# Kernel optimization log

Measured on AMD Instinct MI355X. Metric: run time of the kernel, lower is better.

## Reference

```python
import jax, jax.numpy as jnp
import numpy as np

B, N, D = 256, 196, 1024   # batch, regions, vis_embed_dim
HID, ATT, SIN, WID, ISD = 1024, 256, 1024, 1024, 256
S = 10                      # sentence steps


def _lin(key, out_dim, in_dim):
    kw, kb = jax.random.split(key)
    w = jax.random.normal(kw, (out_dim, in_dim), jnp.float32) * 0.02
    b = jax.random.normal(kb, (out_dim,), jnp.float32) * 0.02
    return w, b


def setup_inputs() -> dict:
    key = jax.random.key(0)
    ks = jax.random.split(key, 16)
    inp = {}
    inp['vis_enc'] = jax.random.normal(ks[0], (B, N, D), jnp.float32)
    inp['sentences'] = jax.random.randint(ks[1], (B, S, 50), 0, 10000, jnp.int64)
    inp['enc_att_w'], inp['enc_att_b'] = _lin(ks[2], ATT, D)
    inp['dec_att_w'], inp['dec_att_b'] = _lin(ks[3], ATT, HID)
    inp['full_att_w'], inp['full_att_b'] = _lin(ks[4], 1, ATT)
    inp['ctx_w'], inp['ctx_b'] = _lin(ks[5], SIN, D)
    inp['W_ih'], inp['b_ih'] = _lin(ks[6], 4 * HID, SIN)
    inp['W_hh'], inp['b_hh'] = _lin(ks[7], 4 * HID, HID)
    inp['topic_hid_w'], inp['topic_hid_b'] = _lin(ks[8], WID, HID)
    inp['topic_ctx_w'], inp['topic_ctx_b'] = _lin(ks[9], WID, SIN)
    inp['stop_prev_w'], inp['stop_prev_b'] = _lin(ks[10], ISD, HID)
    inp['stop_cur_w'], inp['stop_cur_b'] = _lin(ks[11], ISD, HID)
    inp['final_stop_w'], inp['final_stop_b'] = _lin(ks[12], 2, ISD)
    return inp


def reference(vis_enc, sentences,
              enc_att_w, enc_att_b, dec_att_w, dec_att_b, full_att_w, full_att_b,
              ctx_w, ctx_b, W_ih, b_ih, W_hh, b_hh,
              topic_hid_w, topic_hid_b, topic_ctx_w, topic_ctx_b,
              stop_prev_w, stop_prev_b, stop_cur_w, stop_cur_b,
              final_stop_w, final_stop_b):
    batch, hid = vis_enc.shape[0], W_hh.shape[1]
    sent_num = sentences.shape[1]
    # encoder projection is h-independent -> hoist out of the recurrence
    vis_enc_att = jnp.einsum('bnd,ad->bna', vis_enc, enc_att_w) + enc_att_b  # [B,N,ATT]

    def step(carry, _):
        h, c = carry
        # CoAtt additive attention
        dec = h @ dec_att_w.T + dec_att_b                       # [B,ATT]
        join = jnp.tanh(vis_enc_att + dec[:, None, :])          # [B,N,ATT]
        logits = jnp.einsum('bna,a->bn', join, full_att_w[0]) + full_att_b[0]
        scores = jax.nn.softmax(logits, axis=1)                 # [B,N]
        att_out = jnp.einsum('bn,bnd->bd', scores, vis_enc)     # [B,D]
        ctx = att_out @ ctx_w.T + ctx_b                         # [B,SIN]
        h_prev = h
        # LSTMCell
        gates = ctx @ W_ih.T + b_ih + h @ W_hh.T + b_hh         # [B,4H]
        i, f, g, o = jnp.split(gates, 4, axis=1)
        c_new = jax.nn.sigmoid(f) * c + jax.nn.sigmoid(i) * jnp.tanh(g)
        h_new = jax.nn.sigmoid(o) * jnp.tanh(c_new)
        # topic + stop heads
        topic = jnp.tanh(h_new @ topic_hid_w.T + topic_hid_b
                         + ctx @ topic_ctx_w.T + topic_ctx_b)   # [B,WID]
        p = jnp.tanh(h_prev @ stop_prev_w.T + stop_prev_b
                     + h_new @ stop_cur_w.T + stop_cur_b)
        p = p @ final_stop_w.T + final_stop_b                   # [B,2]
        return (h_new, c_new), (topic, p)

    h0 = jnp.zeros((batch, hid), vis_enc.dtype)
    c0 = jnp.zeros((batch, hid), vis_enc.dtype)
    _, (topics, ps) = jax.lax.scan(step, (h0, c0), None, length=sent_num)
    topics = jnp.transpose(topics, (1, 0, 2))  # [B,S,WID]
    ps = jnp.transpose(ps, (1, 0, 2))          # [B,S,2]
    return topics, ps
```

## Files before the change

kernel.cpp:

```cpp
#include <hip/hip_runtime.h>
#include <hip/hip_bf16.h>
#include <math.h>

static constexpr int BB = 256;
static constexpr int NR = 196;
static constexpr int DV = 1024;
static constexpr int HH = 1024;
static constexpr int AT = 256;
static constexpr int SI = 1024;
static constexpr int WI = 1024;
static constexpr int IS = 256;
static constexpr int ST = 10;

__device__ __forceinline__ float sigmoidf_(float x) { return 1.0f / (1.0f + expf(-x)); }

__device__ __forceinline__ ushort f2bf(float x) {
    uint u = __float_as_uint(x);
    return (ushort)((u + 0x7FFFu + ((u >> 16) & 1u)) >> 16);
}
__device__ __forceinline__ float bf2f(ushort b) { return __uint_as_float(((uint)b) << 16); }

using bf16x8 = __attribute__((ext_vector_type(8))) short;
using f32x4  = __attribute__((ext_vector_type(4))) float;
#define MFMA_B16(a, b, c) __builtin_amdgcn_mfma_f32_16x16x32_bf16((a), (b), (c), 0, 0, 0)

__device__ __forceinline__ void split8(const float4& u, const float4& v, uint4& hq, uint4& lq) {
    ushort h0 = f2bf(u.x), h1 = f2bf(u.y), h2 = f2bf(u.z), h3 = f2bf(u.w);
    ushort h4 = f2bf(v.x), h5 = f2bf(v.y), h6 = f2bf(v.z), h7 = f2bf(v.w);
    hq.x = h0 | ((uint)h1 << 16); hq.y = h2 | ((uint)h3 << 16);
    hq.z = h4 | ((uint)h5 << 16); hq.w = h6 | ((uint)h7 << 16);
    ushort l0 = f2bf(u.x - bf2f(h0)), l1 = f2bf(u.y - bf2f(h1));
    ushort l2 = f2bf(u.z - bf2f(h2)), l3 = f2bf(u.w - bf2f(h3));
    ushort l4 = f2bf(v.x - bf2f(h4)), l5 = f2bf(v.y - bf2f(h5));
    ushort l6 = f2bf(v.z - bf2f(h6)), l7 = f2bf(v.w - bf2f(h7));
    lq.x = l0 | ((uint)l1 << 16); lq.y = l2 | ((uint)l3 << 16);
    lq.z = l4 | ((uint)l5 << 16); lq.w = l6 | ((uint)l7 << 16);
}

struct CvtTab { const float* s[9]; ushort* h[9]; ushort* l[9]; };

__global__ __launch_bounds__(256) void convert_split(CvtTab tab) {
    const int cum[10] = {0, 256, 512, 1536, 5632, 9728, 10752, 11776, 12032, 12288};
    const int bid = blockIdx.x;
    int seg = 0;
#pragma unroll
    for (int i = 1; i < 9; ++i) if (bid >= cum[i]) seg = i;
    const float* s = tab.s[seg];
    ushort* h = tab.h[seg];
    ushort* l = tab.l[seg];
    const int r = bid - cum[seg];
    int rd = r;
    if (seg == 3 || seg == 4) rd = (r & 1023) * 4 + (r >> 10);
    const int src = r * 1024 + threadIdx.x * 4;
    const size_t dst = (size_t)rd * 1024 + threadIdx.x * 4;
    float4 v = *(const float4*)(s + src);
    ushort h0 = f2bf(v.x), h1 = f2bf(v.y), h2 = f2bf(v.z), h3 = f2bf(v.w);
    uint2 hq, lq;
    hq.x = h0 | ((uint)h1 << 16); hq.y = h2 | ((uint)h3 << 16);
    ushort l0 = f2bf(v.x - bf2f(h0)), l1 = f2bf(v.y - bf2f(h1));
    ushort l2 = f2bf(v.z - bf2f(h2)), l3 = f2bf(v.w - bf2f(h3));
    lq.x = l0 | ((uint)l1 << 16); lq.y = l2 | ((uint)l3 << 16);
    *(uint2*)(h + dst) = hq;
    *(uint2*)(l + dst) = lq;
}

__global__ __launch_bounds__(256) void convert_vis(
    const float* __restrict__ src, ushort* __restrict__ dst)
{
    const size_t i = ((size_t)blockIdx.x * 256 + threadIdx.x) * 8;
    const float4 v0 = *(const float4*)(src + i);
    const float4 v1 = *(const float4*)(src + i + 4);
    uint4 o;
    o.x = f2bf(v0.x) | ((uint)f2bf(v0.y) << 16);
    o.y = f2bf(v0.z) | ((uint)f2bf(v0.w) << 16);
    o.z = f2bf(v1.x) | ((uint)f2bf(v1.y) << 16);
    o.w = f2bf(v1.z) | ((uint)f2bf(v1.w) << 16);
    *(uint4*)(dst + i) = o;
}

__global__ __launch_bounds__(256) void transpose_split(
    const float* __restrict__ src, ushort* __restrict__ dh, ushort* __restrict__ dl)
{
    __shared__ float T[32][33];
    const int tx = threadIdx.x & 31, ty = threadIdx.x >> 5;
    const int k0 = blockIdx.x * 32, n0 = blockIdx.y * 32;
#pragma unroll
    for (int j = 0; j < 4; ++j)
        T[ty + 8 * j][tx] = src[(size_t)(k0 + ty + 8 * j) * 1024 + n0 + tx];
    __syncthreads();
#pragma unroll
    for (int j = 0; j < 4; ++j) {
        const float v = T[tx][ty + 8 * j];
        const ushort h = f2bf(v);
        const size_t o = (size_t)(n0 + ty + 8 * j) * 1024 + k0 + tx;
        dh[o] = h;
        dl[o] = f2bf(v - bf2f(h));
    }
}

__global__ __launch_bounds__(256) void foldbias(
    const float* __restrict__ W, const float* __restrict__ v,
    const float* __restrict__ b, float* __restrict__ out)
{
    const int n = blockIdx.x * 4 + (threadIdx.x >> 6);
    const int lane = threadIdx.x & 63;
    const float* wr = W + (size_t)n * 1024;
    float p = 0.f;
#pragma unroll
    for (int i = 0; i < 4; ++i) {
        const float4 wv = *(const float4*)&wr[i * 256 + lane * 4];
        const float4 vv = *(const float4*)&v[i * 256 + lane * 4];
        p = fmaf(wv.x, vv.x, p); p = fmaf(wv.y, vv.y, p);
        p = fmaf(wv.z, vv.z, p); p = fmaf(wv.w, vv.w, p);
    }
    for (int off = 32; off; off >>= 1) p += __shfl_down(p, off);
    if (lane == 0) out[n] = p + b[n];
}

template <int ILV>
__global__ __launch_bounds__(256) void mgemm_ws(
    const float* __restrict__ A, const ushort* __restrict__ Wh, const ushort* __restrict__ Wl,
    ushort* __restrict__ Ch, ushort* __restrict__ Cl, int N, int K)
{
    __shared__ __align__(16) ushort SM[4 * 64 * 40];
    ushort* Ah = SM; ushort* Al = SM + 2560; ushort* Bh = SM + 5120; ushort* Bl = SM + 7680;

    const int t = threadIdx.x;
    const int m0 = blockIdx.y * 64, n0 = blockIdx.x * 64;
    const int w = t >> 6, lane = t & 63;
    const int l15 = lane & 15, q = lane >> 4;
    const int sr = t >> 2, sq = (t & 3) * 8;
    const int nch = K >> 5;

    f32x4 acc[4] = {};
    float4 pa0, pa1; uint4 pbh, pbl;
    auto pref = [&](int c) {
        const int k0 = c << 5;
        const float* ap = &A[(size_t)(m0 + sr) * K + k0 + sq];
        pa0 = *(const float4*)ap;
        pa1 = *(const float4*)(ap + 4);
        pbh = *(const uint4*)&Wh[(size_t)(n0 + sr) * K + k0 + sq];
        pbl = *(const uint4*)&Wl[(size_t)(n0 + sr) * K + k0 + sq];
    };
    pref(0);

    for (int c = 0; c < nch; ++c) {
        __syncthreads();
        uint4 hq, lq; split8(pa0, pa1, hq, lq);
        *(uint4*)&Ah[sr * 40 + sq] = hq;
        *(uint4*)&Al[sr * 40 + sq] = lq;
        *(uint4*)&Bh[sr * 40 + sq] = pbh;
        *(uint4*)&Bl[sr * 40 + sq] = pbl;
        __syncthreads();
        if (c + 1 < nch) pref(c + 1);
        const bf16x8 bh = *(const bf16x8*)&Bh[(w * 16 + l15) * 40 + q * 8];
        const bf16x8 bl = *(const bf16x8*)&Bl[(w * 16 + l15) * 40 + q * 8];
#pragma unroll
        for (int mi = 0; mi < 4; ++mi) {
            const bf16x8 ah = *(const bf16x8*)&Ah[(mi * 16 + l15) * 40 + q * 8];
            const bf16x8 al = *(const bf16x8*)&Al[(mi * 16 + l15) * 40 + q * 8];
            acc[mi] = MFMA_B16(ah, bh, acc[mi]);
            acc[mi] = MFMA_B16(ah, bl, acc[mi]);
            acc[mi] = MFMA_B16(al, bh, acc[mi]);
        }
    }

    const int col = n0 + w * 16 + l15;
#pragma unroll
    for (int mi = 0; mi < 4; ++mi) {
#pragma unroll
        for (int j = 0; j < 4; ++j) {
            const int row = m0 + mi * 16 + q * 4 + j;
            const int ro = ILV ? ((row & 1023) * 4 + (row >> 10)) : row;
            const float v = acc[mi][j];
            const ushort h = f2bf(v);
            Ch[(size_t)ro * N + col] = h;
            Cl[(size_t)ro * N + col] = f2bf(v - bf2f(h));
        }
    }
}

template <int EPI, int DUAL, int OMAP>
__global__ __launch_bounds__(256) void mgemm(
    const float* __restrict__ A1, const ushort* __restrict__ W1h, const ushort* __restrict__ W1l,
    const float* __restrict__ b1,
    const float* __restrict__ A2, const ushort* __restrict__ W2h, const ushort* __restrict__ W2l,
    const float* __restrict__ b2,
    float* __restrict__ C, int M, int N, int K, int ldc)
{
    __shared__ __align__(16) ushort SM[4 * 64 * 40];
    ushort* Ah = SM; ushort* Al = SM + 2560; ushort* Bh = SM + 5120; ushort* Bl = SM + 7680;

    const int t = threadIdx.x;
    const int m0 = blockIdx.y * 64, n0 = blockIdx.x * 64;
    const int w = t >> 6, lane = t & 63;
    const int l15 = lane & 15, q = lane >> 4;
    const int sr = t >> 2, sq = (t & 3) * 8;
    const int KC = K >> 5, nch = (DUAL ? 2 : 1) * KC;

    f32x4 acc[4] = {};
    float4 pa0, pa1; uint4 pbh, pbl;

    auto pref = [&](int c) {
        const int pass = DUAL ? (c >= KC ? 1 : 0) : 0;
        const int k0 = (c - pass * KC) << 5;
        const float* A = pass ? A2 : A1;
        const ushort* Wh = pass ? W2h : W1h;
        const ushort* Wl = pass ? W2l : W1l;
        const float* ap = &A[(size_t)(m0 + sr) * K + k0 + sq];
        pa0 = *(const float4*)ap;
        pa1 = *(const float4*)(ap + 4);
        pbh = *(const uint4*)&Wh[(size_t)(n0 + sr) * K + k0 + sq];
        pbl = *(const uint4*)&Wl[(size_t)(n0 + sr) * K + k0 + sq];
    };
    pref(0);

    for (int c = 0; c < nch; ++c) {
        __syncthreads();
        uint4 hq, lq; split8(pa0, pa1, hq, lq);
        *(uint4*)&Ah[sr * 40 + sq] = hq;
        *(uint4*)&Al[sr * 40 + sq] = lq;
        *(uint4*)&Bh[sr * 40 + sq] = pbh;
        *(uint4*)&Bl[sr * 40 + sq] = pbl;
        __syncthreads();
        if (c + 1 < nch) pref(c + 1);
        const bf16x8 bh = *(const bf16x8*)&Bh[(w * 16 + l15) * 40 + q * 8];
        const bf16x8 bl = *(const bf16x8*)&Bl[(w * 16 + l15) * 40 + q * 8];
#pragma unroll
        for (int mi = 0; mi < 4; ++mi) {
            const bf16x8 ah = *(const bf16x8*)&Ah[(mi * 16 + l15) * 40 + q * 8];
            const bf16x8 al = *(const bf16x8*)&Al[(mi * 16 + l15) * 40 + q * 8];
            acc[mi] = MFMA_B16(ah, bh, acc[mi]);
            acc[mi] = MFMA_B16(ah, bl, acc[mi]);
            acc[mi] = MFMA_B16(al, bh, acc[mi]);
        }
    }

    const int col = n0 + w * 16 + l15;
    float bias = b1[col];
    if (DUAL) bias += b2[col];
#pragma unroll
    for (int mi = 0; mi < 4; ++mi) {
#pragma unroll
        for (int j = 0; j < 4; ++j) {
            const int row = m0 + mi * 16 + q * 4 + j;
            float v = acc[mi][j] + bias;
            if (EPI == 1) v = tanhf(v);
            if (OMAP)
                C[((size_t)(row & 255) * ST + (row >> 8)) * ldc + col] = v;
            else
                C[(size_t)row * ldc + col] = v;
        }
    }
}

__global__ __launch_bounds__(512) void mgemm8_lstm(
    const float* __restrict__ A1, const ushort* __restrict__ W1h, const ushort* __restrict__ W1l,
    const float* __restrict__ b1,
    const float* __restrict__ A2, const ushort* __restrict__ W2h, const ushort* __restrict__ W2l,
    const float* __restrict__ b2,
    int K, float* __restrict__ cvec, float* __restrict__ hnew)
{
    __shared__ __align__(16) ushort SM[32256];

    const int t = threadIdx.x;
    const int m0 = blockIdx.y * 64, n0 = blockIdx.x * 32;
    const int w = t >> 6, lane = t & 63;
    const int g = w >> 2, wg = w & 3;
    const int l15 = lane & 15, q = lane >> 4;
    const int tl = t & 255;
    const int sr = tl >> 2, sq4 = (tl & 3) * 16;
    const int br = tl >> 3, bq = (tl & 7) * 8;
    const int mh = wg >> 1;
    const int colL = (wg & 1) * 16 + l15;

    ushort* Ah = SM + g * 13824;
    ushort* Al = Ah + 4608;
    ushort* Bh = Al + 4608;
    ushort* Bl = Bh + 2304;

    const int nchg = K >> 6;
    const float*  A  = g ? A2 : A1;
    const ushort* Wh = g ? W2h : W1h;
    const ushort* Wl = g ? W2l : W1l;

    f32x4 acc[2] = {};
    float4 pa0, pa1, pa2, pa3; uint4 pbh, pbl;
    auto pref = [&](int c) {
        const int k0 = c << 6;
        const float* ap = &A[(size_t)(m0 + sr) * K + k0 + sq4];
        pa0 = *(const float4*)ap;       pa1 = *(const float4*)(ap + 4);
        pa2 = *(const float4*)(ap + 8); pa3 = *(const float4*)(ap + 12);
        pbh = *(const uint4*)&Wh[(size_t)(n0 + br) * K + k0 + bq];
        pbl = *(const uint4*)&Wl[(size_t)(n0 + br) * K + k0 + bq];
    };
    pref(0);

    for (int c = 0; c < nchg; ++c) {
        __syncthreads();
        uint4 hq, lq;
        split8(pa0, pa1, hq, lq);
        *(uint4*)&Ah[sr * 72 + sq4] = hq;
        *(uint4*)&Al[sr * 72 + sq4] = lq;
        split8(pa2, pa3, hq, lq);
        *(uint4*)&Ah[sr * 72 + sq4 + 8] = hq;
        *(uint4*)&Al[sr * 72 + sq4 + 8] = lq;
        *(uint4*)&Bh[br * 72 + bq] = pbh;
        *(uint4*)&Bl[br * 72 + bq] = pbl;
        __syncthreads();
        if (c + 1 < nchg) pref(c + 1);
#pragma unroll
        for (int ks = 0; ks < 2; ++ks) {
            const bf16x8 bh = *(const bf16x8*)&Bh[colL * 72 + ks * 32 + q * 8];
            const bf16x8 bl = *(const bf16x8*)&Bl[colL * 72 + ks * 32 + q * 8];
#pragma unroll
            for (int i = 0; i < 2; ++i) {
                const int mi = mh * 2 + i;
                const bf16x8 ah = *(const bf16x8*)&Ah[(mi * 16 + l15) * 72 + ks * 32 + q * 8];
                const bf16x8 al = *(const bf16x8*)&Al[(mi * 16 + l15) * 72 + ks * 32 + q * 8];
                acc[i] = MFMA_B16(ah, bh, acc[i]);
                acc[i] = MFMA_B16(ah, bl, acc[i]);
                acc[i] = MFMA_B16(al, bh, acc[i]);
            }
        }
    }

    float* comb = (float*)(SM + 27648);
    __syncthreads();
    if (g == 1) {
#pragma unroll
        for (int i = 0; i < 2; ++i)
#pragma unroll
            for (int j = 0; j < 4; ++j) comb[tl * 9 + i * 4 + j] = acc[i][j];
    }
    __syncthreads();
    if (g == 0) {
#pragma unroll
        for (int i = 0; i < 2; ++i)
#pragma unroll
            for (int j = 0; j < 4; ++j) acc[i][j] += comb[tl * 9 + i * 4 + j];
    }

    float* G = (float*)(SM + 13824);
    if (g == 0) {
        const int colG = n0 + colL;
        const int gate = colG & 3, unit = colG >> 2;
        const float bias = b1[gate * 1024 + unit] + b2[gate * 1024 + unit];
#pragma unroll
        for (int i = 0; i < 2; ++i) {
            const int mi = mh * 2 + i;
#pragma unroll
            for (int j = 0; j < 4; ++j)
                G[(mi * 16 + q * 4 + j) * 40 + colL] = acc[i][j] + bias;
        }
    }
    __syncthreads();
    {
        const int row = t >> 3, ul = t & 7;
        const float4 g4 = *(const float4*)&G[row * 40 + ul * 4];
        const size_t ci = (size_t)(m0 + row) * HH + (n0 >> 2) + ul;
        const float cn = sigmoidf_(g4.y) * cvec[ci] + sigmoidf_(g4.x) * tanhf(g4.z);
        cvec[ci] = cn;
        hnew[ci] = sigmoidf_(g4.w) * tanhf(cn);
    }
}

__global__ __launch_bounds__(256) void mgemm_preb(
    const ushort* __restrict__ vh, const ushort* __restrict__ Wh, const ushort* __restrict__ Wl,
    const float* __restrict__ bias, ushort* __restrict__ C)
{
    __shared__ __align__(16) ushort Avh[64 * 40];
    __shared__ __align__(16) ushort Bh[256 * 40];
    __shared__ __align__(16) ushort Bl[256 * 40];

    const int t = threadIdx.x;
    const int m0 = blockIdx.x * 64;
    const int w = t >> 6, lane = t & 63;
    const int l15 = lane & 15, q = lane >> 4;
    const int ar = t >> 2, ac = (t & 3) * 8;
    const int K = DV;

    f32x4 acc[4][4] = {};

    for (int c = 0; c < 32; ++c) {
        const int k0 = c << 5;
        __syncthreads();
        *(uint4*)&Avh[ar * 40 + ac] = *(const uint4*)&vh[(size_t)(m0 + ar) * K + k0 + ac];
#pragma unroll
        for (int j = 0; j < 4; ++j) {
            const int r = j * 64 + (t >> 2);
            *(uint4*)&Bh[r * 40 + ac] = *(const uint4*)&Wh[(size_t)r * K + k0 + ac];
            *(uint4*)&Bl[r * 40 + ac] = *(const uint4*)&Wl[(size_t)r * K + k0 + ac];
        }
        __syncthreads();

        bf16x8 ah[4];
#pragma unroll
        for (int mi = 0; mi < 4; ++mi)
            ah[mi] = *(const bf16x8*)&Avh[(mi * 16 + l15) * 40 + q * 8];
#pragma unroll
        for (int ni = 0; ni < 4; ++ni) {
            const bf16x8 bh = *(const bf16x8*)&Bh[(w * 64 + ni * 16 + l15) * 40 + q * 8];
            const bf16x8 bl = *(const bf16x8*)&Bl[(w * 64 + ni * 16 + l15) * 40 + q * 8];
#pragma unroll
            for (int mi = 0; mi < 4; ++mi) {
                acc[mi][ni] = MFMA_B16(ah[mi], bh, acc[mi][ni]);
                acc[mi][ni] = MFMA_B16(ah[mi], bl, acc[mi][ni]);
            }
        }
    }

#pragma unroll
    for (int ni = 0; ni < 4; ++ni) {
        const int col = w * 64 + ni * 16 + l15;
        const float bb = bias[col];
#pragma unroll
        for (int mi = 0; mi < 4; ++mi)
#pragma unroll
            for (int j = 0; j < 4; ++j) {
                const int row = m0 + mi * 16 + q * 4 + j;
                C[(size_t)row * AT + col] = f2bf(acc[mi][ni][j] + bb);
            }
    }
}

__global__ __launch_bounds__(256) void mgemm_pre(
    const float* __restrict__ A, const ushort* __restrict__ Wh, const ushort* __restrict__ Wl,
    const float* __restrict__ bias, ushort* __restrict__ C)
{
    __shared__ __align__(16) ushort Ah[64 * 40], Al[64 * 40];
    __shared__ __align__(16) ushort Bh[256 * 40], Bl[256 * 40];

    const int t = threadIdx.x;
    const int m0 = blockIdx.x * 64;
    const int w = t >> 6, lane = t & 63;
    const int l15 = lane & 15, q = lane >> 4;
    const int sr = t >> 2, sq = (t & 3) * 8;
    const int K = DV;

    f32x4 acc[4][4] = {};
    float4 pa0, pa1;
    auto prefA = [&](int k0) {
        const float* ap = &A[(size_t)(m0 + sr) * K + k0 + sq];
        pa0 = *(const float4*)ap;
        pa1 = *(const float4*)(ap + 4);
    };
    prefA(0);

    for (int c = 0; c < 32; ++c) {
        const int k0 = c << 5;
        __syncthreads();
        uint4 hq, lq; split8(pa0, pa1, hq, lq);
        *(uint4*)&Ah[sr * 40 + sq] = hq;
        *(uint4*)&Al[sr * 40 + sq] = lq;
#pragma unroll
        for (int i = 0; i < 4; ++i) {
            const int r = sr + 64 * i;
            *(uint4*)&Bh[r * 40 + sq] = *(const uint4*)&Wh[(size_t)r * K + k0 + sq];
            *(uint4*)&Bl[r * 40 + sq] = *(const uint4*)&Wl[(size_t)r * K + k0 + sq];
        }
        __syncthreads();
        if (c + 1 < 32) prefA((c + 1) << 5);

        bf16x8 ah[4], al[4];
#pragma unroll
        for (int mi = 0; mi < 4; ++mi) {
            ah[mi] = *(const bf16x8*)&Ah[(mi * 16 + l15) * 40 + q * 8];
            al[mi] = *(const bf16x8*)&Al[(mi * 16 + l15) * 40 + q * 8];
        }
#pragma unroll
        for (int ni = 0; ni < 4; ++ni) {
            const bf16x8 bh = *(const bf16x8*)&Bh[(w * 64 + ni * 16 + l15) * 40 + q * 8];
            const bf16x8 bl = *(const bf16x8*)&Bl[(w * 64 + ni * 16 + l15) * 40 + q * 8];
#pragma unroll
            for (int mi = 0; mi < 4; ++mi) {
                acc[mi][ni] = MFMA_B16(ah[mi], bh, acc[mi][ni]);
                acc[mi][ni] = MFMA_B16(ah[mi], bl, acc[mi][ni]);
                acc[mi][ni] = MFMA_B16(al[mi], bh, acc[mi][ni]);
            }
        }
    }

#pragma unroll
    for (int ni = 0; ni < 4; ++ni) {
        const int col = w * 64 + ni * 16 + l15;
        const float bb = bias[col];
#pragma unroll
        for (int mi = 0; mi < 4; ++mi)
#pragma unroll
            for (int j = 0; j < 4; ++j) {
                const int row = m0 + mi * 16 + q * 4 + j;
                C[(size_t)row * AT + col] = f2bf(acc[mi][ni][j] + bb);
            }
    }
}

template <int VBF>
__global__ __launch_bounds__(1024) void att_step(
    const ushort* __restrict__ vis_att, const float* __restrict__ h,
    const float* __restrict__ dec_w, const float* __restrict__ dec_b,
    const float* __restrict__ fw, const float* __restrict__ fbp,
    const void* __restrict__ visp, float* __restrict__ att_out)
{
    const int b = blockIdx.x;
    const int t = threadIdx.x;
    const int lane = t & 63;
    const int w = t >> 6;

    __shared__ float hs[HH];
    __shared__ float decs[AT];
    __shared__ float fwv[AT];
    __shared__ float logit[NR + 4];
    __shared__ float sc[NR + 4];
    __shared__ float red[8];
    __shared__ float part[8][DV];

    hs[t] = h[(size_t)b * HH + t];
    if (t < AT) fwv[t] = fw[t];
    __syncthreads();
    const float fb = fbp[0];

#pragma unroll
    for (int j = 0; j < 16; ++j) {
        const int a = w * 16 + j;
        const float* wr = dec_w + (size_t)a * HH;
        float p = 0.f;
#pragma unroll
        for (int i = 0; i < 4; ++i) {
            const float4 wv = *(const float4*)&wr[i * 256 + lane * 4];
            const float4 hv = *(const float4*)&hs[i * 256 + lane * 4];
            p = fmaf(wv.x, hv.x, p); p = fmaf(wv.y, hv.y, p);
            p = fmaf(wv.z, hv.z, p); p = fmaf(wv.w, hv.w, p);
        }
        for (int off = 32; off; off >>= 1) p += __shfl_down(p, off);
        if (lane == 0) decs[a] = p + dec_b[a];
    }
    __syncthreads();

    for (int n = w; n < NR; n += 16) {
        const ushort4 v4 = *(const ushort4*)&vis_att[((size_t)b * NR + n) * AT + lane * 4];
        const int a = lane * 4;
        float s = tanhf(bf2f(v4.x) + decs[a]) * fwv[a];
        s = fmaf(tanhf(bf2f(v4.y) + decs[a + 1]), fwv[a + 1], s);
        s = fmaf(tanhf(bf2f(v4.z) + decs[a + 2]), fwv[a + 2], s);
        s = fmaf(tanhf(bf2f(v4.w) + decs[a + 3]), fwv[a + 3], s);
        for (int off = 32; off; off >>= 1) s += __shfl_down(s, off);
        if (lane == 0) logit[n] = s + fb;
    }
    __syncthreads();

    float m = -1e30f, e = 0.f;
    if (t < NR) m = logit[t];
    if (t < 256) {
        for (int off = 32; off; off >>= 1) m = fmaxf(m, __shfl_down(m, off));
        if (lane == 0) red[w] = m;
    }
    __syncthreads();
    m = fmaxf(fmaxf(red[0], red[1]), fmaxf(red[2], red[3]));
    if (t < NR) e = expf(logit[t] - m);
    if (t < 256) {
        float ss = e;
        for (int off = 32; off; off >>= 1) ss += __shfl_down(ss, off);
        if (lane == 0) red[4 + w] = ss;
    }
    __syncthreads();
    const float S = red[4] + red[5] + red[6] + red[7];
    if (t < NR) sc[t] = e / S;
    __syncthreads();

    const int slice = t >> 7;
    const int c8 = (t & 127) * 8;
    const int nbeg = (slice <= 4) ? 25 * slice : 100 + 24 * (slice - 4);
    const int nend = (slice < 4) ? nbeg + 25 : nbeg + 24;
    float a0 = 0.f, a1 = 0.f, a2 = 0.f, a3 = 0.f;
    float a4 = 0.f, a5 = 0.f, a6 = 0.f, a7 = 0.f;
    if (VBF) {
        const ushort* vb = (const ushort*)visp + (size_t)b * NR * DV + c8;
        for (int n = nbeg; n < nend; ++n) {
            const float s = sc[n];
            const uint4 v = *(const uint4*)&vb[(size_t)n * DV];
            a0 = fmaf(s, bf2f((ushort)(v.x & 0xFFFF)), a0);
            a1 = fmaf(s, bf2f((ushort)(v.x >> 16)), a1);
            a2 = fmaf(s, bf2f((ushort)(v.y & 0xFFFF)), a2);
            a3 = fmaf(s, bf2f((ushort)(v.y >> 16)), a3);
            a4 = fmaf(s, bf2f((ushort)(v.z & 0xFFFF)), a4);
            a5 = fmaf(s, bf2f((ushort)(v.z >> 16)), a5);
            a6 = fmaf(s, bf2f((ushort)(v.w & 0xFFFF)), a6);
            a7 = fmaf(s, bf2f((ushort)(v.w >> 16)), a7);
        }
    } else {
        const float* vb = (const float*)visp + (size_t)b * NR * DV + c8;
        for (int n = nbeg; n < nend; ++n) {
            const float s = sc[n];
            const float4 v0 = *(const float4*)&vb[(size_t)n * DV];
            const float4 v1 = *(const float4*)&vb[(size_t)n * DV + 4];
            a0 = fmaf(s, v0.x, a0); a1 = fmaf(s, v0.y, a1);
            a2 = fmaf(s, v0.z, a2); a3 = fmaf(s, v0.w, a3);
            a4 = fmaf(s, v1.x, a4); a5 = fmaf(s, v1.y, a5);
            a6 = fmaf(s, v1.z, a6); a7 = fmaf(s, v1.w, a7);
        }
    }
    float4 av0; av0.x = a0; av0.y = a1; av0.z = a2; av0.w = a3;
    float4 av1; av1.x = a4; av1.y = a5; av1.z = a6; av1.w = a7;
    *(float4*)&part[slice][c8]     = av0;
    *(float4*)&part[slice][c8 + 4] = av1;
    __syncthreads();
    att_out[(size_t)b * DV + t] = ((part[0][t] + part[1][t]) + (part[2][t] + part[3][t]))
                                + ((part[4][t] + part[5][t]) + (part[6][t] + part[7][t]));
}

__global__ __launch_bounds__(256) void stop_final_all(
    const float* __restrict__ pt, const float* __restrict__ fw,
    const float* __restrict__ fb, float* __restrict__ outp)
{
    const int row = blockIdx.x;
    const int s = row >> 8, b = row & 255;
    const int t = threadIdx.x;
    const int lane = t & 63;
    const int w = t >> 6;

    __shared__ float red[16];
    const float v = pt[(size_t)row * IS + t];
    float p0 = v * fw[t];
    float p1 = v * fw[IS + t];
    for (int off = 32; off; off >>= 1) {
        p0 += __shfl_down(p0, off);
        p1 += __shfl_down(p1, off);
    }
    if (lane == 0) { red[w] = p0; red[8 + w] = p1; }
    __syncthreads();
    if (t == 0) {
        outp[((size_t)b * ST + s) * 2 + 0] = red[0] + red[1] + red[2] + red[3] + fb[0];
        outp[((size_t)b * ST + s) * 2 + 1] = red[8] + red[9] + red[10] + red[11] + fb[1];
    }
}

extern "C" void kernel_launch(void* const* d_in, const int* in_sizes, int n_in,
                              void* d_out, int out_size, void* d_ws, size_t ws_size,
                              hipStream_t stream)
{
    const float* vis        = (const float*)d_in[0];
    const float* enc_att_w  = (const float*)d_in[2];
    const float* enc_att_b  = (const float*)d_in[3];
    const float* dec_att_w  = (const float*)d_in[4];
    const float* dec_att_b  = (const float*)d_in[5];
    const float* full_att_w = (const float*)d_in[6];
    const float* full_att_b = (const float*)d_in[7];
    const float* ctx_w      = (const float*)d_in[8];
    const float* ctx_b      = (const float*)d_in[9];
    const float* W_ih       = (const float*)d_in[10];
    const float* b_ih       = (const float*)d_in[11];
    const float* W_hh       = (const float*)d_in[12];
    const float* b_hh       = (const float*)d_in[13];
    const float* topic_hid_w = (const float*)d_in[14];
    const float* topic_hid_b = (const float*)d_in[15];
    const float* topic_ctx_w = (const float*)d_in[16];
    const float* topic_ctx_b = (const float*)d_in[17];
    const float* stop_prev_w = (const float*)d_in[18];
    const float* stop_prev_b = (const float*)d_in[19];
    const float* stop_cur_w  = (const float*)d_in[20];
    const float* stop_cur_b  = (const float*)d_in[21];
    const float* final_stop_w = (const float*)d_in[22];
    const float* final_stop_b = (const float*)d_in[23];

    float* out_topics = (float*)d_out;
    float* out_ps     = (float*)d_out + (size_t)BB * ST * WI;

    char* ws = (char*)d_ws;
    size_t off = 0;
    auto alloc = [&](size_t bytes) -> void* {
        void* p = (void*)(ws + off);
        off += (bytes + 255) & ~(size_t)255;
        return p;
    };
    ushort* vis_att = (ushort*)alloc((size_t)BB * NR * AT * 2);
    const size_t WTOT = 12582912;
    ushort* wh = (ushort*)alloc(WTOT * 2);
    ushort* wl = (ushort*)alloc(WTOT * 2);
    float* h_all   = (float*)alloc((size_t)(ST + 1) * BB * HH * 4);
    float* att_all = (float*)alloc((size_t)ST * BB * DV * 4);
    float* cbuf    = (float*)alloc((size_t)BB * HH * 4);
    float* pt_all  = (float*)alloc((size_t)ST * BB * IS * 4);
    ushort* ctT_h  = (ushort*)alloc((size_t)SI * DV * 2);
    ushort* ctT_l  = (ushort*)alloc((size_t)SI * DV * 2);
    ushort* cmb_h  = (ushort*)alloc((size_t)4 * HH * SI * 2);
    ushort* cmb_l  = (ushort*)alloc((size_t)4 * HH * SI * 2);
    ushort* tcc_h  = (ushort*)alloc((size_t)WI * SI * 2);
    ushort* tcc_l  = (ushort*)alloc((size_t)WI * SI * 2);
    float* bf_ih   = (float*)alloc((size_t)4 * HH * 4);
    float* bf_tc   = (float*)alloc((size_t)WI * 4);
    if (off > ws_size) return;
    ushort* vis_bf = nullptr;
    {
        const size_t need = (size_t)BB * NR * DV * 2;
        if (off + need <= ws_size) vis_bf = (ushort*)alloc(need);
    }

    const size_t O_ENC = 0;
    const size_t O_DEC = 262144;
    const size_t O_CTX = 524288;
    const size_t O_IH  = 1572864;
    const size_t O_HH  = 5767168;
    const size_t O_TH  = 9961472;
    const size_t O_TC  = 11010048;
    const size_t O_SP  = 12058624;
    const size_t O_SC  = 12320768;

    CvtTab tab;
    const float* srcs[9] = {enc_att_w, dec_att_w, ctx_w, W_ih, W_hh,
                            topic_hid_w, topic_ctx_w, stop_prev_w, stop_cur_w};
    const size_t offs[9] = {O_ENC, O_DEC, O_CTX, O_IH, O_HH, O_TH, O_TC, O_SP, O_SC};
    for (int i = 0; i < 9; ++i) {
        tab.s[i] = srcs[i];
        tab.h[i] = wh + offs[i];
        tab.l[i] = wl + offs[i];
    }

    hipMemsetAsync(h_all, 0, (size_t)BB * HH * 4, stream);
    hipMemsetAsync(cbuf, 0, (size_t)BB * HH * 4, stream);

    convert_split<<<12288, 256, 0, stream>>>(tab);

    transpose_split<<<dim3(SI / 32, DV / 32), 256, 0, stream>>>(ctx_w, ctT_h, ctT_l);
    mgemm_ws<1><<<dim3(SI / 64, 4 * HH / 64), 256, 0, stream>>>(
        W_ih, ctT_h, ctT_l, cmb_h, cmb_l, SI, DV);
    mgemm_ws<0><<<dim3(SI / 64, WI / 64), 256, 0, stream>>>(
        topic_ctx_w, ctT_h, ctT_l, tcc_h, tcc_l, SI, DV);
    foldbias<<<(4 * HH) / 4, 256, 0, stream>>>(W_ih, ctx_b, b_ih, bf_ih);
    foldbias<<<WI / 4, 256, 0, stream>>>(topic_ctx_w, ctx_b, topic_ctx_b, bf_tc);

    if (vis_bf) {
        convert_vis<<<(BB * NR * DV) / (256 * 8), 256, 0, stream>>>(vis, vis_bf);
        mgemm_preb<<<(BB * NR) / 64, 256, 0, stream>>>(
            vis_bf, wh + O_ENC, wl + O_ENC, enc_att_b, vis_att);
    } else {
        mgemm_pre<<<(BB * NR) / 64, 256, 0, stream>>>(
            vis, wh + O_ENC, wl + O_ENC, enc_att_b, vis_att);
    }

    for (int s = 0; s < ST; ++s) {
        float* hc = h_all + (size_t)s * BB * HH;
        float* hn = h_all + (size_t)(s + 1) * BB * HH;
        float* atts = att_all + (size_t)s * BB * DV;
        if (vis_bf)
            att_step<1><<<BB, 1024, 0, stream>>>(vis_att, hc, dec_att_w, dec_att_b,
                                                 full_att_w, full_att_b, vis_bf, atts);
        else
            att_step<0><<<BB, 1024, 0, stream>>>(vis_att, hc, dec_att_w, dec_att_b,
                                                 full_att_w, full_att_b, vis, atts);
        mgemm8_lstm<<<dim3(4 * HH / 32, BB / 64), 512, 0, stream>>>(
            atts, cmb_h, cmb_l, bf_ih,
            hc, wh + O_HH, wl + O_HH, b_hh,
            SI, cbuf, hn);
    }

    mgemm<1, 1, 1><<<dim3(WI / 64, (ST * BB) / 64), 256, 0, stream>>>(
        h_all + (size_t)BB * HH, wh + O_TH, wl + O_TH, topic_hid_b,
        att_all, tcc_h, tcc_l, bf_tc,
        out_topics, ST * BB, WI, HH, WI);
    mgemm<1, 1, 0><<<dim3(IS / 64, (ST * BB) / 64), 256, 0, stream>>>(
        h_all, wh + O_SP, wl + O_SP, stop_prev_b,
        h_all + (size_t)BB * HH, wh + O_SC, wl + O_SC, stop_cur_b,
        pt_all, ST * BB, IS, HH, IS);
    stop_final_all<<<ST * BB, 256, 0, stream>>>(pt_all, final_stop_w, final_stop_b, out_ps);
}
```

Measured before the change: 1.168 ms.

## Convert only needed weights and shrink LSTM GEMM K-chunk to cut LDS

The bf16 hi/lo split-conversion pass now covers only the five weight matrices still used directly (enc_att, W_hh, topic_hid, stop_prev, stop_cur), dropping dec_att, ctx, W_ih and topic_ctx, which are folded or unused. This reduces conversion traffic and workspace size. Separately, the fused LSTM GEMM kernel now stages 32-wide K chunks instead of 64, shrinking shared memory per block, likely to raise occupancy at the cost of twice as many barrier iterations.

```diff
diff --git a/kernel.cpp b/kernel.cpp
--- a/kernel.cpp
+++ b/kernel.cpp
@@ -37,20 +37,20 @@
     lq.z = l4 | ((uint)l5 << 16); lq.w = l6 | ((uint)l7 << 16);
 }
 
-struct CvtTab { const float* s[9]; ushort* h[9]; ushort* l[9]; };
+struct CvtTab { const float* s[5]; ushort* h[5]; ushort* l[5]; };
 
 __global__ __launch_bounds__(256) void convert_split(CvtTab tab) {
-    const int cum[10] = {0, 256, 512, 1536, 5632, 9728, 10752, 11776, 12032, 12288};
+    const int cum[6] = {0, 256, 4352, 5376, 5632, 5888};
     const int bid = blockIdx.x;
     int seg = 0;
 #pragma unroll
-    for (int i = 1; i < 9; ++i) if (bid >= cum[i]) seg = i;
+    for (int i = 1; i < 5; ++i) if (bid >= cum[i]) seg = i;
     const float* s = tab.s[seg];
     ushort* h = tab.h[seg];
     ushort* l = tab.l[seg];
     const int r = bid - cum[seg];
     int rd = r;
-    if (seg == 3 || seg == 4) rd = (r & 1023) * 4 + (r >> 10);
+    if (seg == 1) rd = (r & 1023) * 4 + (r >> 10);
     const int src = r * 1024 + threadIdx.x * 4;
     const size_t dst = (size_t)rd * 1024 + threadIdx.x * 4;
     float4 v = *(const float4*)(s + src);
@@ -261,7 +261,7 @@
     const float* __restrict__ b2,
     int K, float* __restrict__ cvec, float* __restrict__ hnew)
 {
-    __shared__ __align__(16) ushort SM[32256];
+    __shared__ __align__(16) ushort SM[20480];
 
     const int t = threadIdx.x;
     const int m0 = blockIdx.y * 64, n0 = blockIdx.x * 32;
@@ -269,63 +269,56 @@
     const int g = w >> 2, wg = w & 3;
     const int l15 = lane & 15, q = lane >> 4;
     const int tl = t & 255;
-    const int sr = tl >> 2, sq4 = (tl & 3) * 16;
-    const int br = tl >> 3, bq = (tl & 7) * 8;
+    const int sr = tl >> 2, sq = (tl & 3) * 8;
+    const int br = tl >> 3, bq = (tl & 7) * 4;
     const int mh = wg >> 1;
     const int colL = (wg & 1) * 16 + l15;
 
-    ushort* Ah = SM + g * 13824;
-    ushort* Al = Ah + 4608;
-    ushort* Bh = Al + 4608;
-    ushort* Bl = Bh + 2304;
-
-    const int nchg = K >> 6;
+    ushort* Ah = SM + g * 7680;
+    ushort* Al = Ah + 2560;
+    ushort* Bh = Al + 2560;
+    ushort* Bl = Bh + 1280;
+
+    const int nchg = K >> 5;
     const float*  A  = g ? A2 : A1;
     const ushort* Wh = g ? W2h : W1h;
     const ushort* Wl = g ? W2l : W1l;
 
     f32x4 acc[2] = {};
-    float4 pa0, pa1, pa2, pa3; uint4 pbh, pbl;
+    float4 pa0, pa1; uint2 pbh, pbl;
     auto pref = [&](int c) {
-        const int k0 = c << 6;
-        const float* ap = &A[(size_t)(m0 + sr) * K + k0 + sq4];
-        pa0 = *(const float4*)ap;       pa1 = *(const float4*)(ap + 4);
-        pa2 = *(const float4*)(ap + 8); pa3 = *(const float4*)(ap + 12);
-        pbh = *(const uint4*)&Wh[(size_t)(n0 + br) * K + k0 + bq];
-        pbl = *(const uint4*)&Wl[(size_t)(n0 + br) * K + k0 + bq];
+        const int k0 = c << 5;
+        const float* ap = &A[(size_t)(m0 + sr) * K + k0 + sq];
+        pa0 = *(const float4*)ap;
+        pa1 = *(const float4*)(ap + 4);
+        pbh = *(const uint2*)&Wh[(size_t)(n0 + br) * K + k0 + bq];
+        pbl = *(const uint2*)&Wl[(size_t)(n0 + br) * K + k0 + bq];
     };
     pref(0);
 
     for (int c = 0; c < nchg; ++c) {
         __syncthreads();
-        uint4 hq, lq;
-        split8(pa0, pa1, hq, lq);
-        *(uint4*)&Ah[sr * 72 + sq4] = hq;
-        *(uint4*)&Al[sr * 72 + sq4] = lq;
-        split8(pa2, pa3, hq, lq);
-        *(uint4*)&Ah[sr * 72 + sq4 + 8] = hq;
-        *(uint4*)&Al[sr * 72 + sq4 + 8] = lq;
-        *(uint4*)&Bh[br * 72 + bq] = pbh;
-        *(uint4*)&Bl[br * 72 + bq] = pbl;
+        uint4 hq, lq; split8(pa0, pa1, hq, lq);
+        *(uint4*)&Ah[sr * 40 + sq] = hq;
+        *(uint4*)&Al[sr * 40 + sq] = lq;
+        *(uint2*)&Bh[br * 40 + bq] = pbh;
+        *(uint2*)&Bl[br * 40 + bq] = pbl;
         __syncthreads();
         if (c + 1 < nchg) pref(c + 1);
-#pragma unroll
-        for (int ks = 0; ks < 2; ++ks) {
-            const bf16x8 bh = *(const bf16x8*)&Bh[colL * 72 + ks * 32 + q * 8];
-            const bf16x8 bl = *(const bf16x8*)&Bl[colL * 72 + ks * 32 + q * 8];
-#pragma unroll
-            for (int i = 0; i < 2; ++i) {
-                const int mi = mh * 2 + i;
-                const bf16x8 ah = *(const bf16x8*)&Ah[(mi * 16 + l15) * 72 + ks * 32 + q * 8];
-                const bf16x8 al = *(const bf16x8*)&Al[(mi * 16 + l15) * 72 + ks * 32 + q * 8];
-                acc[i] = MFMA_B16(ah, bh, acc[i]);
-                acc[i] = MFMA_B16(ah, bl, acc[i]);
-                acc[i] = MFMA_B16(al, bh, acc[i]);
-            }
-        }
-    }
-
-    float* comb = (float*)(SM + 27648);
+        const bf16x8 bh = *(const bf16x8*)&Bh[colL * 40 + q * 8];
+        const bf16x8 bl = *(const bf16x8*)&Bl[colL * 40 + q * 8];
+#pragma unroll
+        for (int i = 0; i < 2; ++i) {
+            const int mi = mh * 2 + i;
+            const bf16x8 ah = *(const bf16x8*)&Ah[(mi * 16 + l15) * 40 + q * 8];
+            const bf16x8 al = *(const bf16x8*)&Al[(mi * 16 + l15) * 40 + q * 8];
+            acc[i] = MFMA_B16(ah, bh, acc[i]);
+            acc[i] = MFMA_B16(ah, bl, acc[i]);
+            acc[i] = MFMA_B16(al, bh, acc[i]);
+        }
+    }
+
+    float* comb = (float*)(SM + 15360);
     __syncthreads();
     if (g == 1) {
 #pragma unroll
@@ -341,7 +334,7 @@
             for (int j = 0; j < 4; ++j) acc[i][j] += comb[tl * 9 + i * 4 + j];
     }
 
-    float* G = (float*)(SM + 13824);
+    float* G = (float*)(SM + 7680);
     if (g == 0) {
         const int colG = n0 + colL;
         const int gate = colG & 3, unit = colG >> 2;
@@ -674,7 +667,7 @@
         return p;
     };
     ushort* vis_att = (ushort*)alloc((size_t)BB * NR * AT * 2);
-    const size_t WTOT = 12582912;
+    const size_t WTOT = (size_t)5888 * 1024;
     ushort* wh = (ushort*)alloc(WTOT * 2);
     ushort* wl = (ushort*)alloc(WTOT * 2);
     float* h_all   = (float*)alloc((size_t)(ST + 1) * BB * HH * 4);
@@ -697,20 +690,15 @@
     }
 
     const size_t O_ENC = 0;
-    const size_t O_DEC = 262144;
-    const size_t O_CTX = 524288;
-    const size_t O_IH  = 1572864;
-    const size_t O_HH  = 5767168;
-    const size_t O_TH  = 9961472;
-    const size_t O_TC  = 11010048;
-    const size_t O_SP  = 12058624;
-    const size_t O_SC  = 12320768;
+    const size_t O_HH  = 262144;
+    const size_t O_TH  = 4456448;
+    const size_t O_SP  = 5505024;
+    const size_t O_SC  = 5767168;
 
     CvtTab tab;
-    const float* srcs[9] = {enc_att_w, dec_att_w, ctx_w, W_ih, W_hh,
-                            topic_hid_w, topic_ctx_w, stop_prev_w, stop_cur_w};
-    const size_t offs[9] = {O_ENC, O_DEC, O_CTX, O_IH, O_HH, O_TH, O_TC, O_SP, O_SC};
-    for (int i = 0; i < 9; ++i) {
+    const float* srcs[5] = {enc_att_w, W_hh, topic_hid_w, stop_prev_w, stop_cur_w};
+    const size_t offs[5] = {O_ENC, O_HH, O_TH, O_SP, O_SC};
+    for (int i = 0; i < 5; ++i) {
         tab.s[i] = srcs[i];
         tab.h[i] = wh + offs[i];
         tab.l[i] = wl + offs[i];
@@ -719,7 +707,7 @@
     hipMemsetAsync(h_all, 0, (size_t)BB * HH * 4, stream);
     hipMemsetAsync(cbuf, 0, (size_t)BB * HH * 4, stream);
 
-    convert_split<<<12288, 256, 0, stream>>>(tab);
+    convert_split<<<5888, 256, 0, stream>>>(tab);
 
     transpose_split<<<dim3(SI / 32, DV / 32), 256, 0, stream>>>(ctx_w, ctT_h, ctT_l);
     mgemm_ws<1><<<dim3(SI / 64, 4 * HH / 64), 256, 0, stream>>>(
```

Result: slower. 1.199 ms (+2.6%).

## Pre-split LSTM activations into bf16 hi/lo in producers and trim weight conversion

Applied to the files above, without the earlier changes.

The attention step and the LSTM epilogue now write bf16 hi/lo splits of their outputs, so the LSTM GEMM loads pre-split operands instead of reading fp32 and splitting inside its inner loop. The weight conversion pass also drops the matrices that are no longer read in split form (dec_att, ctx, W_ih, topic_ctx), which shrinks that launch. This removes per-tile conversion ALU work and halves the A-operand load width in the recurrent GEMM. In exchange the producers do extra conversion and global stores, and the kernel needs extra buffers plus memsets.

```diff
diff --git a/kernel.cpp b/kernel.cpp
--- a/kernel.cpp
+++ b/kernel.cpp
@@ -37,20 +37,20 @@
     lq.z = l4 | ((uint)l5 << 16); lq.w = l6 | ((uint)l7 << 16);
 }
 
-struct CvtTab { const float* s[9]; ushort* h[9]; ushort* l[9]; };
+struct CvtTab { const float* s[5]; ushort* h[5]; ushort* l[5]; };
 
 __global__ __launch_bounds__(256) void convert_split(CvtTab tab) {
-    const int cum[10] = {0, 256, 512, 1536, 5632, 9728, 10752, 11776, 12032, 12288};
+    const int cum[6] = {0, 256, 4352, 5376, 5632, 5888};
     const int bid = blockIdx.x;
     int seg = 0;
 #pragma unroll
-    for (int i = 1; i < 9; ++i) if (bid >= cum[i]) seg = i;
+    for (int i = 1; i < 5; ++i) if (bid >= cum[i]) seg = i;
     const float* s = tab.s[seg];
     ushort* h = tab.h[seg];
     ushort* l = tab.l[seg];
     const int r = bid - cum[seg];
     int rd = r;
-    if (seg == 3 || seg == 4) rd = (r & 1023) * 4 + (r >> 10);
+    if (seg == 1) rd = (r & 1023) * 4 + (r >> 10);
     const int src = r * 1024 + threadIdx.x * 4;
     const size_t dst = (size_t)rd * 1024 + threadIdx.x * 4;
     float4 v = *(const float4*)(s + src);
@@ -255,11 +255,14 @@
 }
 
 __global__ __launch_bounds__(512) void mgemm8_lstm(
-    const float* __restrict__ A1, const ushort* __restrict__ W1h, const ushort* __restrict__ W1l,
+    const ushort* __restrict__ A1h, const ushort* __restrict__ A1l,
+    const ushort* __restrict__ W1h, const ushort* __restrict__ W1l,
     const float* __restrict__ b1,
-    const float* __restrict__ A2, const ushort* __restrict__ W2h, const ushort* __restrict__ W2l,
+    const ushort* __restrict__ A2h, const ushort* __restrict__ A2l,
+    const ushort* __restrict__ W2h, const ushort* __restrict__ W2l,
     const float* __restrict__ b2,
-    int K, float* __restrict__ cvec, float* __restrict__ hnew)
+    int K, float* __restrict__ cvec, float* __restrict__ hnew,
+    ushort* __restrict__ hnh, ushort* __restrict__ hnl)
 {
     __shared__ __align__(16) ushort SM[32256];
 
@@ -280,17 +283,20 @@
     ushort* Bl = Bh + 2304;
 
     const int nchg = K >> 6;
-    const float*  A  = g ? A2 : A1;
-    const ushort* Wh = g ? W2h : W1h;
-    const ushort* Wl = g ? W2l : W1l;
+    const ushort* Ahg = g ? A2h : A1h;
+    const ushort* Alg = g ? A2l : A1l;
+    const ushort* Wh  = g ? W2h : W1h;
+    const ushort* Wl  = g ? W2l : W1l;
 
     f32x4 acc[2] = {};
-    float4 pa0, pa1, pa2, pa3; uint4 pbh, pbl;
+    uint4 pah0, pah1, pal0, pal1, pbh, pbl;
     auto pref = [&](int c) {
         const int k0 = c << 6;
-        const float* ap = &A[(size_t)(m0 + sr) * K + k0 + sq4];
-        pa0 = *(const float4*)ap;       pa1 = *(const float4*)(ap + 4);
-        pa2 = *(const float4*)(ap + 8); pa3 = *(const float4*)(ap + 12);
+        const size_t ab = (size_t)(m0 + sr) * K + k0 + sq4;
+        pah0 = *(const uint4*)&Ahg[ab];
+        pah1 = *(const uint4*)&Ahg[ab + 8];
+        pal0 = *(const uint4*)&Alg[ab];
+        pal1 = *(const uint4*)&Alg[ab + 8];
         pbh = *(const uint4*)&Wh[(size_t)(n0 + br) * K + k0 + bq];
         pbl = *(const uint4*)&Wl[(size_t)(n0 + br) * K + k0 + bq];
     };
@@ -298,13 +304,10 @@
 
     for (int c = 0; c < nchg; ++c) {
         __syncthreads();
-        uint4 hq, lq;
-        split8(pa0, pa1, hq, lq);
-        *(uint4*)&Ah[sr * 72 + sq4] = hq;
-        *(uint4*)&Al[sr * 72 + sq4] = lq;
-        split8(pa2, pa3, hq, lq);
-        *(uint4*)&Ah[sr * 72 + sq4 + 8] = hq;
-        *(uint4*)&Al[sr * 72 + sq4 + 8] = lq;
+        *(uint4*)&Ah[sr * 72 + sq4]     = pah0;
+        *(uint4*)&Ah[sr * 72 + sq4 + 8] = pah1;
+        *(uint4*)&Al[sr * 72 + sq4]     = pal0;
+        *(uint4*)&Al[sr * 72 + sq4 + 8] = pal1;
         *(uint4*)&Bh[br * 72 + bq] = pbh;
         *(uint4*)&Bl[br * 72 + bq] = pbl;
         __syncthreads();
@@ -361,7 +364,11 @@
         const size_t ci = (size_t)(m0 + row) * HH + (n0 >> 2) + ul;
         const float cn = sigmoidf_(g4.y) * cvec[ci] + sigmoidf_(g4.x) * tanhf(g4.z);
         cvec[ci] = cn;
-        hnew[ci] = sigmoidf_(g4.w) * tanhf(cn);
+        const float hv = sigmoidf_(g4.w) * tanhf(cn);
+        hnew[ci] = hv;
+        const ushort hhi = f2bf(hv);
+        hnh[ci] = hhi;
+        hnl[ci] = f2bf(hv - bf2f(hhi));
     }
 }
 
@@ -500,7 +507,8 @@
     const ushort* __restrict__ vis_att, const float* __restrict__ h,
     const float* __restrict__ dec_w, const float* __restrict__ dec_b,
     const float* __restrict__ fw, const float* __restrict__ fbp,
-    const void* __restrict__ visp, float* __restrict__ att_out)
+    const void* __restrict__ visp, float* __restrict__ att_out,
+    ushort* __restrict__ att_h, ushort* __restrict__ att_l)
 {
     const int b = blockIdx.x;
     const int t = threadIdx.x;
@@ -605,8 +613,12 @@
     *(float4*)&part[slice][c8]     = av0;
     *(float4*)&part[slice][c8 + 4] = av1;
     __syncthreads();
-    att_out[(size_t)b * DV + t] = ((part[0][t] + part[1][t]) + (part[2][t] + part[3][t]))
-                                + ((part[4][t] + part[5][t]) + (part[6][t] + part[7][t]));
+    const float v = ((part[0][t] + part[1][t]) + (part[2][t] + part[3][t]))
+                  + ((part[4][t] + part[5][t]) + (part[6][t] + part[7][t]));
+    att_out[(size_t)b * DV + t] = v;
+    const ushort vh16 = f2bf(v);
+    att_h[(size_t)b * DV + t] = vh16;
+    att_l[(size_t)b * DV + t] = f2bf(v - bf2f(vh16));
 }
 
 __global__ __launch_bounds__(256) void stop_final_all(
@@ -674,11 +686,15 @@
         return p;
     };
     ushort* vis_att = (ushort*)alloc((size_t)BB * NR * AT * 2);
-    const size_t WTOT = 12582912;
+    const size_t WTOT = (size_t)5888 * 1024;
     ushort* wh = (ushort*)alloc(WTOT * 2);
     ushort* wl = (ushort*)alloc(WTOT * 2);
     float* h_all   = (float*)alloc((size_t)(ST + 1) * BB * HH * 4);
+    ushort* hh_h   = (ushort*)alloc((size_t)(ST + 1) * BB * HH * 2);
+    ushort* hh_l   = (ushort*)alloc((size_t)(ST + 1) * BB * HH * 2);
     float* att_all = (float*)alloc((size_t)ST * BB * DV * 4);
+    ushort* att_h  = (ushort*)alloc((size_t)BB * DV * 2);
+    ushort* att_l  = (ushort*)alloc((size_t)BB * DV * 2);
     float* cbuf    = (float*)alloc((size_t)BB * HH * 4);
     float* pt_all  = (float*)alloc((size_t)ST * BB * IS * 4);
     ushort* ctT_h  = (ushort*)alloc((size_t)SI * DV * 2);
@@ -697,29 +713,26 @@
     }
 
     const size_t O_ENC = 0;
-    const size_t O_DEC = 262144;
-    const size_t O_CTX = 524288;
-    const size_t O_IH  = 1572864;
-    const size_t O_HH  = 5767168;
-    const size_t O_TH  = 9961472;
-    const size_t O_TC  = 11010048;
-    const size_t O_SP  = 12058624;
-    const size_t O_SC  = 12320768;
+    const size_t O_HH  = 262144;
+    const size_t O_TH  = 4456448;
+    const size_t O_SP  = 5505024;
+    const size_t O_SC  = 5767168;
 
     CvtTab tab;
-    const float* srcs[9] = {enc_att_w, dec_att_w, ctx_w, W_ih, W_hh,
-                            topic_hid_w, topic_ctx_w, stop_prev_w, stop_cur_w};
-    const size_t offs[9] = {O_ENC, O_DEC, O_CTX, O_IH, O_HH, O_TH, O_TC, O_SP, O_SC};
-    for (int i = 0; i < 9; ++i) {
+    const float* srcs[5] = {enc_att_w, W_hh, topic_hid_w, stop_prev_w, stop_cur_w};
+    const size_t offs[5] = {O_ENC, O_HH, O_TH, O_SP, O_SC};
+    for (int i = 0; i < 5; ++i) {
         tab.s[i] = srcs[i];
         tab.h[i] = wh + offs[i];
         tab.l[i] = wl + offs[i];
     }
 
     hipMemsetAsync(h_all, 0, (size_t)BB * HH * 4, stream);
+    hipMemsetAsync(hh_h, 0, (size_t)BB * HH * 2, stream);
+    hipMemsetAsync(hh_l, 0, (size_t)BB * HH * 2, stream);
     hipMemsetAsync(cbuf, 0, (size_t)BB * HH * 4, stream);
 
-    convert_split<<<12288, 256, 0, stream>>>(tab);
+    convert_split<<<5888, 256, 0, stream>>>(tab);
 
     transpose_split<<<dim3(SI / 32, DV / 32), 256, 0, stream>>>(ctx_w, ctT_h, ctT_l);
     mgemm_ws<1><<<dim3(SI / 64, 4 * HH / 64), 256, 0, stream>>>(
@@ -741,17 +754,23 @@
     for (int s = 0; s < ST; ++s) {
         float* hc = h_all + (size_t)s * BB * HH;
         float* hn = h_all + (size_t)(s + 1) * BB * HH;
+        ushort* hch = hh_h + (size_t)s * BB * HH;
+        ushort* hcl = hh_l + (size_t)s * BB * HH;
+        ushort* hnh = hh_h + (size_t)(s + 1) * BB * HH;
+        ushort* hnl = hh_l + (size_t)(s + 1) * BB * HH;
         float* atts = att_all + (size_t)s * BB * DV;
         if (vis_bf)
             att_step<1><<<BB, 1024, 0, stream>>>(vis_att, hc, dec_att_w, dec_att_b,
-                                                 full_att_w, full_att_b, vis_bf, atts);
+                                                 full_att_w, full_att_b, vis_bf, atts,
+                                                 att_h, att_l);
         else
             att_step<0><<<BB, 1024, 0, stream>>>(vis_att, hc, dec_att_w, dec_att_b,
-                                                 full_att_w, full_att_b, vis, atts);
+                                                 full_att_w, full_att_b, vis, atts,
+                                                 att_h, att_l);
         mgemm8_lstm<<<dim3(4 * HH / 32, BB / 64), 512, 0, stream>>>(
-            atts, cmb_h, cmb_l, bf_ih,
-            hc, wh + O_HH, wl + O_HH, b_hh,
-            SI, cbuf, hn);
+            att_h, att_l, cmb_h, cmb_l, bf_ih,
+            hch, hcl, wh + O_HH, wl + O_HH, b_hh,
+            SI, cbuf, hn, hnh, hnl);
     }
 
     mgemm<1, 1, 1><<<dim3(WI / 64, (ST * BB) / 64), 256, 0, stream>>>(
```

New measurement: 1.099 ms. 6.0% less time.
